# Performance work log

Hardware: AMD Instinct MI355X
Metric: run time of the kernel (lower is better)

The kernel has to match this reference:

```python
import jax, jax.numpy as jnp
import numpy as np

FP8_E4M3_MAX = 448.0  # max finite value of float8_e4m3fn
SCALE = 2.0           # hardcoded activation scale in FP8QDQLinear.__init__
WEIGHT_SCALE = 2.0    # hardcoded weight scale


def quantize_fp8(x, scale):
    # torchao quantize_affine_float8: divide by scale, saturate to fp8 range, cast
    return jnp.clip(x / scale, -FP8_E4M3_MAX, FP8_E4M3_MAX).astype(jnp.float8_e4m3fn)


def dequantize_fp8(q, scale):
    # torchao dequantize_affine_float8: upcast to fp32 then multiply by scale
    return q.astype(jnp.float32) * scale


def setup_inputs() -> dict:
    key = jax.random.key(0)
    k1, k2, k3 = jax.random.split(key, 3)
    in_features, out_features = 4096, 4096
    inp = jax.random.normal(k1, (4, 4096, in_features), dtype=jnp.float32)
    # weight is created as randn().to(float8_e4m3fn) in __init__ (a buffer, not a Parameter)
    weight = jax.random.normal(k2, (out_features, in_features), dtype=jnp.float32).astype(jnp.float8_e4m3fn)
    bias = jax.random.normal(k3, (out_features,), dtype=jnp.float32)
    return {"input": inp, "weight": weight, "bias": bias}


def reference(input, weight, bias):
    # dequantize fp8 weight
    w = dequantize_fp8(weight, WEIGHT_SCALE)            # [O, I] fp32
    # QDQ fake-quant on activations
    dq_input = dequantize_fp8(quantize_fp8(input, SCALE), SCALE)  # [B, S, I]
    # standard linear: y = x @ W^T + b
    out = jnp.einsum('bsi,oi->bso', dq_input, w) + bias
    return out
```

## Files before the change

kernel.cpp:

```cpp
#include <hip/hip_runtime.h>

typedef float f32x4 __attribute__((ext_vector_type(4)));
typedef float f32x16 __attribute__((ext_vector_type(16)));
typedef int i32x4 __attribute__((ext_vector_type(4)));
typedef int i32x8 __attribute__((ext_vector_type(8)));

#define M_DIM 16384L
#define N_DIM 4096L
#define K_DIM 4096L

__device__ __forceinline__ unsigned int f32_to_e4m3(float x, float scale) {
  float v = fminf(fmaxf(x * scale, -448.f), 448.f);
  unsigned int u = __float_as_uint(v);
  unsigned int s = (u >> 24) & 0x80u;
  float ax = fabsf(v);
  unsigned int ua = __float_as_uint(ax);
  unsigned int subn = (unsigned int)rintf(ax * 512.0f);
  unsigned int r = ua + 0x7FFFFu + ((ua >> 20) & 1u);
  unsigned int nrm = ((r >> 20) & 0x7FFu) - 960u;
  unsigned int mag = (ax < 0.015625f) ? subn : nrm;
  return mag | s;
}

__device__ __forceinline__ unsigned int pack4_e4m3(float4 v, float scale) {
  return f32_to_e4m3(v.x, scale) | (f32_to_e4m3(v.y, scale) << 8) |
         (f32_to_e4m3(v.z, scale) << 16) | (f32_to_e4m3(v.w, scale) << 24);
}

__global__ __launch_bounds__(256) void quant_fp8(const float* __restrict__ in,
                                                 unsigned int* __restrict__ out,
                                                 float scale) {
  const long i = (long)blockIdx.x * 256 + threadIdx.x;
  out[i] = pack4_e4m3(reinterpret_cast<const float4*>(in)[i], scale);
}

__device__ __forceinline__ void gld_lds16(const unsigned char* g, unsigned char* l) {
  __builtin_amdgcn_global_load_lds(
      (const __attribute__((address_space(1))) unsigned int*)g,
      (__attribute__((address_space(3))) unsigned int*)l,
      16, 0, 0);
}

__device__ __forceinline__ uint4 quant16(const float* p, float scale) {
  const float4* q = reinterpret_cast<const float4*>(p);
  uint4 r;
  r.x = pack4_e4m3(q[0], scale);
  r.y = pack4_e4m3(q[1], scale);
  r.z = pack4_e4m3(q[2], scale);
  r.w = pack4_e4m3(q[3], scale);
  return r;
}

template <bool FA, bool FB>
__global__ __launch_bounds__(256) void gemm_fp8(const unsigned char* __restrict__ A8,
                                                const float* __restrict__ Af,
                                                const unsigned char* __restrict__ B8,
                                                const float* __restrict__ Bf,
                                                const float* __restrict__ bias,
                                                float* __restrict__ C) {
  __shared__ unsigned char sA[128 * 64];
  __shared__ unsigned char sB[128 * 64];

  const int t = threadIdx.x;
  const int lane = t & 63;
  const int w = t >> 6;
  const int wm = w >> 1;
  const int wn = w & 1;
  const long bx = blockIdx.x;
  const long by = blockIdx.y;

  f32x16 acc[2][2] = {};

  const int l0 = w * 64 + lane;
  const int l1 = l0 + 256;
  const int r0 = l0 >> 2, c0 = (l0 & 3) ^ ((l0 >> 3) & 3);
  const int r1 = l1 >> 2, c1 = (l1 & 3) ^ ((l1 >> 3) & 3);

  const unsigned char* gA0 = nullptr; const unsigned char* gA1 = nullptr;
  const float* fA0 = nullptr;         const float* fA1 = nullptr;
  if constexpr (FA) {
    fA0 = Af + (by * 128 + r0) * K_DIM + c0 * 16;
    fA1 = Af + (by * 128 + r1) * K_DIM + c1 * 16;
  } else {
    gA0 = A8 + (by * 128 + r0) * K_DIM + c0 * 16;
    gA1 = A8 + (by * 128 + r1) * K_DIM + c1 * 16;
  }
  const unsigned char* gB0 = nullptr; const unsigned char* gB1 = nullptr;
  const float* fB0 = nullptr;         const float* fB1 = nullptr;
  if constexpr (FB) {
    fB0 = Bf + (bx * 128 + r0) * K_DIM + c0 * 16;
    fB1 = Bf + (bx * 128 + r1) * K_DIM + c1 * 16;
  } else {
    gB0 = B8 + (bx * 128 + r0) * K_DIM + c0 * 16;
    gB1 = B8 + (bx * 128 + r1) * K_DIM + c1 * 16;
  }

  unsigned char* lA0 = sA + w * 1024;
  unsigned char* lA1 = sA + 4096 + w * 1024;
  unsigned char* lB0 = sB + w * 1024;
  unsigned char* lB1 = sB + 4096 + w * 1024;

  const int r32 = lane & 31;
  const int key = (lane >> 1) & 3;
  const int p_lo = ((lane >> 5) << 1) ^ key;
  const unsigned char* sAw = sA + wm * 4096;
  const unsigned char* sBw = sB + wn * 4096;

  for (int kt = 0; kt < (int)(K_DIM / 64); ++kt) {
    if constexpr (FA) {
      *reinterpret_cast<uint4*>(sA + l0 * 16) = quant16(fA0, 0.5f);
      *reinterpret_cast<uint4*>(sA + l1 * 16) = quant16(fA1, 0.5f);
      fA0 += 64; fA1 += 64;
    } else {
      gld_lds16(gA0, lA0);
      gld_lds16(gA1, lA1);
      gA0 += 64; gA1 += 64;
    }
    if constexpr (FB) {
      *reinterpret_cast<uint4*>(sB + l0 * 16) = quant16(fB0, 1.0f);
      *reinterpret_cast<uint4*>(sB + l1 * 16) = quant16(fB1, 1.0f);
      fB0 += 64; fB1 += 64;
    } else {
      gld_lds16(gB0, lB0);
      gld_lds16(gB1, lB1);
      gB0 += 64; gB1 += 64;
    }
    __syncthreads();

    i32x8 af[2], bf[2];
#pragma unroll
    for (int i = 0; i < 2; ++i) {
      const unsigned char* pa = sAw + (i * 32 + r32) * 64;
      i32x4 alo = *reinterpret_cast<const i32x4*>(pa + p_lo * 16);
      i32x4 ahi = *reinterpret_cast<const i32x4*>(pa + (p_lo ^ 1) * 16);
      af[i] = i32x8{alo[0], alo[1], alo[2], alo[3], ahi[0], ahi[1], ahi[2], ahi[3]};
      const unsigned char* pb = sBw + (i * 32 + r32) * 64;
      i32x4 blo = *reinterpret_cast<const i32x4*>(pb + p_lo * 16);
      i32x4 bhi = *reinterpret_cast<const i32x4*>(pb + (p_lo ^ 1) * 16);
      bf[i] = i32x8{blo[0], blo[1], blo[2], blo[3], bhi[0], bhi[1], bhi[2], bhi[3]};
    }

#pragma unroll
    for (int i = 0; i < 2; ++i) {
#pragma unroll
      for (int j = 0; j < 2; ++j) {
        acc[i][j] = __builtin_amdgcn_mfma_scale_f32_32x32x64_f8f6f4(
            af[i], bf[j], acc[i][j], 0, 0, 0, 0x7F7F7F7F, 0, 0x7F7F7F7F);
      }
    }
    __syncthreads();
  }

  const int mrow = 4 * (lane >> 5);
  const long gm_base = by * 128 + wm * 64;
  const long gn_base = bx * 128 + wn * 64 + r32;
#pragma unroll
  for (int nj = 0; nj < 2; ++nj) {
    const long gn = gn_base + nj * 32;
    const float bv = bias[gn];
#pragma unroll
    for (int mi = 0; mi < 2; ++mi) {
#pragma unroll
      for (int r = 0; r < 16; ++r) {
        const long gm = gm_base + mi * 32 + (r & 3) + 8 * (r >> 2) + mrow;
        C[gm * N_DIM + gn] = acc[mi][nj][r] * 4.0f + bv;
      }
    }
  }
}

extern "C" void kernel_launch(void* const* d_in, const int* in_sizes, int n_in,
                              void* d_out, int out_size, void* d_ws, size_t ws_size,
                              hipStream_t stream) {
  const float* inp = (const float*)d_in[0];
  const float* wgt = (const float*)d_in[1];
  const float* bias = (const float*)d_in[2];
  float* out = (float*)d_out;

  dim3 grid((unsigned)(N_DIM / 128), (unsigned)(M_DIM / 128));
  const size_t A_BYTES = (size_t)(M_DIM * K_DIM);
  const size_t B_BYTES = (size_t)(N_DIM * K_DIM);

  if (ws_size >= A_BYTES + B_BYTES) {
    unsigned char* aq = (unsigned char*)d_ws;
    unsigned char* wq = (unsigned char*)d_ws + A_BYTES;
    quant_fp8<<<dim3((unsigned)(M_DIM * K_DIM / 1024)), dim3(256), 0, stream>>>(
        inp, (unsigned int*)aq, 0.5f);
    quant_fp8<<<dim3((unsigned)(N_DIM * K_DIM / 1024)), dim3(256), 0, stream>>>(
        wgt, (unsigned int*)wq, 1.0f);
    gemm_fp8<false, false><<<grid, dim3(256), 0, stream>>>(aq, nullptr, wq, nullptr, bias, out);
  } else if (ws_size >= B_BYTES) {
    unsigned char* wq = (unsigned char*)d_ws;
    quant_fp8<<<dim3((unsigned)(N_DIM * K_DIM / 1024)), dim3(256), 0, stream>>>(
        wgt, (unsigned int*)wq, 1.0f);
    gemm_fp8<true, false><<<grid, dim3(256), 0, stream>>>(nullptr, inp, wq, nullptr, bias, out);
  } else {
    gemm_fp8<true, true><<<grid, dim3(256), 0, stream>>>(nullptr, inp, nullptr, wgt, bias, out);
  }
}
```

Before: 772.3 us.

## Add 256x256-tile triple-buffered FP8 GEMM with interleaved loads and block swizzle

Introduces a new GEMM kernel with 256x256 output tiles, 8 waves per block, and a 3-stage LDS ring buffer. Global-to-LDS prefetches for future K steps are interleaved between MFMA groups, using explicit vmcnt waits, barriers and setprio. Block indices are swizzled for L2 locality. The goal is to raise data reuse per tile and hide memory latency behind MFMA work. In exchange it uses 96KB of LDS and more accumulator registers per thread, which may limit occupancy.

```diff
diff --git a/kernel.cpp b/kernel.cpp
--- a/kernel.cpp
+++ b/kernel.cpp
@@ -51,13 +51,143 @@
   return r;
 }
 
+__device__ __forceinline__ i32x8 ldfrag(const unsigned char* p, int p_lo) {
+  i32x4 lo = *reinterpret_cast<const i32x4*>(p + p_lo * 16);
+  i32x4 hi = *reinterpret_cast<const i32x4*>(p + (p_lo ^ 1) * 16);
+  return i32x8{lo[0], lo[1], lo[2], lo[3], hi[0], hi[1], hi[2], hi[3]};
+}
+
+#define MFMA_SC(a, b, c) \
+  __builtin_amdgcn_mfma_scale_f32_32x32x64_f8f6f4((a), (b), (c), 0, 0, 0, 0x7F7F7F7F, 0, 0x7F7F7F7F)
+
+#define BARRIER() asm volatile("s_barrier" ::: "memory")
+
+__global__ __launch_bounds__(512, 2) void gemm_fp8_256(
+    const unsigned char* __restrict__ A8, const unsigned char* __restrict__ B8,
+    const float* __restrict__ bias, float* __restrict__ C) {
+  __shared__ unsigned char sA[3 * 16384];
+  __shared__ unsigned char sB[3 * 16384];
+
+  const int t = threadIdx.x;
+  const int lane = t & 63;
+  const int w = t >> 6;
+  const int wm = w >> 2;
+  const int wn = w & 3;
+
+  const int bid = (int)blockIdx.y * 16 + (int)blockIdx.x;
+  const int swz = (bid & 7) * 128 + (bid >> 3);
+  const long bx = swz & 15;
+  const long by = swz >> 4;
+
+  f32x16 acc[4][2] = {};
+
+  const int sr = t >> 2;
+  const int sc = (t & 3) ^ ((t >> 3) & 3);
+  const unsigned char* srcA0 = A8 + (by * 256 + sr) * K_DIM + sc * 16 + 128;
+  const unsigned char* srcA1 = A8 + (by * 256 + 128 + sr) * K_DIM + sc * 16 + 128;
+  const unsigned char* srcB0 = B8 + (bx * 256 + sr) * K_DIM + sc * 16 + 128;
+  const unsigned char* srcB1 = B8 + (bx * 256 + 128 + sr) * K_DIM + sc * 16 + 128;
+  const int wofs = w * 1024;
+
+  const int r32 = lane & 31;
+  const int key = (lane >> 1) & 3;
+  const int p_lo = ((lane >> 5) << 1) ^ key;
+  const int arow = wm * 128 + r32;
+  const int brow = wn * 64 + r32;
+
+  gld_lds16(srcA0 - 128, sA + wofs);
+  gld_lds16(srcA1 - 128, sA + 8192 + wofs);
+  gld_lds16(srcB0 - 128, sB + wofs);
+  gld_lds16(srcB1 - 128, sB + 8192 + wofs);
+  gld_lds16(srcA0 - 64, sA + 16384 + wofs);
+  gld_lds16(srcA1 - 64, sA + 16384 + 8192 + wofs);
+  gld_lds16(srcB0 - 64, sB + 16384 + wofs);
+  gld_lds16(srcB1 - 64, sB + 16384 + 8192 + wofs);
+  asm volatile("s_waitcnt vmcnt(4)" ::: "memory");
+  BARRIER();
+
+  int b = 0;
+  for (int kt = 0; kt < 64; ++kt) {
+    int b2 = b + 2;
+    if (b2 >= 3) b2 -= 3;
+    const unsigned char* sAb = sA + b * 16384;
+    const unsigned char* sBb = sB + b * 16384;
+    unsigned char* dA = sA + b2 * 16384 + wofs;
+    unsigned char* dB = sB + b2 * 16384 + wofs;
+    const bool st = kt < 62;
+
+    i32x8 bf0 = ldfrag(sBb + brow * 64, p_lo);
+    i32x8 bf1 = ldfrag(sBb + (brow + 32) * 64, p_lo);
+    i32x8 af = ldfrag(sAb + arow * 64, p_lo);
+    if (st) gld_lds16(srcA0, dA);
+    BARRIER();
+    __builtin_amdgcn_s_setprio(1);
+    acc[0][0] = MFMA_SC(af, bf0, acc[0][0]);
+    acc[0][1] = MFMA_SC(af, bf1, acc[0][1]);
+    __builtin_amdgcn_s_setprio(0);
+    BARRIER();
+
+    af = ldfrag(sAb + (arow + 32) * 64, p_lo);
+    if (st) gld_lds16(srcA1, dA + 8192);
+    BARRIER();
+    __builtin_amdgcn_s_setprio(1);
+    acc[1][0] = MFMA_SC(af, bf0, acc[1][0]);
+    acc[1][1] = MFMA_SC(af, bf1, acc[1][1]);
+    __builtin_amdgcn_s_setprio(0);
+    BARRIER();
+
+    af = ldfrag(sAb + (arow + 64) * 64, p_lo);
+    if (st) gld_lds16(srcB0, dB);
+    BARRIER();
+    __builtin_amdgcn_s_setprio(1);
+    acc[2][0] = MFMA_SC(af, bf0, acc[2][0]);
+    acc[2][1] = MFMA_SC(af, bf1, acc[2][1]);
+    __builtin_amdgcn_s_setprio(0);
+    BARRIER();
+
+    af = ldfrag(sAb + (arow + 96) * 64, p_lo);
+    if (st) gld_lds16(srcB1, dB + 8192);
+    BARRIER();
+    __builtin_amdgcn_s_setprio(1);
+    acc[3][0] = MFMA_SC(af, bf0, acc[3][0]);
+    acc[3][1] = MFMA_SC(af, bf1, acc[3][1]);
+    __builtin_amdgcn_s_setprio(0);
+    if (st) {
+      asm volatile("s_waitcnt vmcnt(4)" ::: "memory");
+    } else {
+      asm volatile("s_waitcnt vmcnt(0)" ::: "memory");
+    }
+    BARRIER();
+
+    srcA0 += 64; srcA1 += 64; srcB0 += 64; srcB1 += 64;
+    if (++b == 3) b = 0;
+  }
+
+  const int mrow = 4 * (lane >> 5);
+  const long gm_base = by * 256 + wm * 128;
+  const long gn_base = bx * 256 + wn * 64 + r32;
+#pragma unroll
+  for (int nj = 0; nj < 2; ++nj) {
+    const long gn = gn_base + nj * 32;
+    const float bv = bias[gn];
+#pragma unroll
+    for (int mi = 0; mi < 4; ++mi) {
+#pragma unroll
+      for (int r = 0; r < 16; ++r) {
+        const long gm = gm_base + mi * 32 + (r & 3) + 8 * (r >> 2) + mrow;
+        C[gm * N_DIM + gn] = acc[mi][nj][r] * 4.0f + bv;
+      }
+    }
+  }
+}
+
 template <bool FA, bool FB>
-__global__ __launch_bounds__(256) void gemm_fp8(const unsigned char* __restrict__ A8,
-                                                const float* __restrict__ Af,
-                                                const unsigned char* __restrict__ B8,
-                                                const float* __restrict__ Bf,
-                                                const float* __restrict__ bias,
-                                                float* __restrict__ C) {
+__global__ __launch_bounds__(256) void gemm_fp8_fb(const unsigned char* __restrict__ A8,
+                                                   const float* __restrict__ Af,
+                                                   const unsigned char* __restrict__ B8,
+                                                   const float* __restrict__ Bf,
+                                                   const float* __restrict__ bias,
+                                                   float* __restrict__ C) {
   __shared__ unsigned char sA[128 * 64];
   __shared__ unsigned char sB[128 * 64];
 
@@ -130,22 +260,15 @@
     i32x8 af[2], bf[2];
 #pragma unroll
     for (int i = 0; i < 2; ++i) {
-      const unsigned char* pa = sAw + (i * 32 + r32) * 64;
-      i32x4 alo = *reinterpret_cast<const i32x4*>(pa + p_lo * 16);
-      i32x4 ahi = *reinterpret_cast<const i32x4*>(pa + (p_lo ^ 1) * 16);
-      af[i] = i32x8{alo[0], alo[1], alo[2], alo[3], ahi[0], ahi[1], ahi[2], ahi[3]};
-      const unsigned char* pb = sBw + (i * 32 + r32) * 64;
-      i32x4 blo = *reinterpret_cast<const i32x4*>(pb + p_lo * 16);
-      i32x4 bhi = *reinterpret_cast<const i32x4*>(pb + (p_lo ^ 1) * 16);
-      bf[i] = i32x8{blo[0], blo[1], blo[2], blo[3], bhi[0], bhi[1], bhi[2], bhi[3]};
+      af[i] = ldfrag(sAw + (i * 32 + r32) * 64, p_lo);
+      bf[i] = ldfrag(sBw + (i * 32 + r32) * 64, p_lo);
     }
 
 #pragma unroll
     for (int i = 0; i < 2; ++i) {
 #pragma unroll
       for (int j = 0; j < 2; ++j) {
-        acc[i][j] = __builtin_amdgcn_mfma_scale_f32_32x32x64_f8f6f4(
-            af[i], bf[j], acc[i][j], 0, 0, 0, 0x7F7F7F7F, 0, 0x7F7F7F7F);
+        acc[i][j] = MFMA_SC(af[i], bf[j], acc[i][j]);
       }
     }
     __syncthreads();
@@ -177,7 +300,6 @@
   const float* bias = (const float*)d_in[2];
   float* out = (float*)d_out;
 
-  dim3 grid((unsigned)(N_DIM / 128), (unsigned)(M_DIM / 128));
   const size_t A_BYTES = (size_t)(M_DIM * K_DIM);
   const size_t B_BYTES = (size_t)(N_DIM * K_DIM);
 
@@ -188,13 +310,15 @@
         inp, (unsigned int*)aq, 0.5f);
     quant_fp8<<<dim3((unsigned)(N_DIM * K_DIM / 1024)), dim3(256), 0, stream>>>(
         wgt, (unsigned int*)wq, 1.0f);
-    gemm_fp8<false, false><<<grid, dim3(256), 0, stream>>>(aq, nullptr, wq, nullptr, bias, out);
+    gemm_fp8_256<<<dim3(16, 64), dim3(512), 0, stream>>>(aq, wq, bias, out);
   } else if (ws_size >= B_BYTES) {
     unsigned char* wq = (unsigned char*)d_ws;
     quant_fp8<<<dim3((unsigned)(N_DIM * K_DIM / 1024)), dim3(256), 0, stream>>>(
         wgt, (unsigned int*)wq, 1.0f);
-    gemm_fp8<true, false><<<grid, dim3(256), 0, stream>>>(nullptr, inp, wq, nullptr, bias, out);
+    gemm_fp8_fb<true, false><<<dim3((unsigned)(N_DIM / 128), (unsigned)(M_DIM / 128)),
+                               dim3(256), 0, stream>>>(nullptr, inp, wq, nullptr, bias, out);
   } else {
-    gemm_fp8<true, true><<<grid, dim3(256), 0, stream>>>(nullptr, inp, nullptr, wgt, bias, out);
-  }
-}
+    gemm_fp8_fb<true, true><<<dim3((unsigned)(N_DIM / 128), (unsigned)(M_DIM / 128)),
+                              dim3(256), 0, stream>>>(nullptr, inp, nullptr, wgt, bias, out);
+  }
+}
```

New measurement: 820.5 us. 1.06x slower.
